# Optimization experiments

Hardware: AMD Instinct MI355X
Metric: run time of the kernel (lower is better)

Reference implementation:

```python
import jax, jax.numpy as jnp
import numpy as np

D_MODEL = 1024
NHEAD = 16
D_FF = 4096
LN_EPS = 1e-5


def _layer_norm(x, g, b):
    mu = jnp.mean(x, axis=-1, keepdims=True)
    var = jnp.mean(jnp.square(x - mu), axis=-1, keepdims=True)
    return (x - mu) * jax.lax.rsqrt(var + LN_EPS) * g + b


def setup_inputs() -> dict:
    key = jax.random.key(0)
    ks = jax.random.split(key, 12)
    d, f = D_MODEL, D_FF
    s = 1.0 / np.sqrt(d)
    inp = {
        "src": jax.random.normal(ks[0], (2, 2048, d), dtype=jnp.float32),
        "Wq": jax.random.uniform(ks[1], (d, d), jnp.float32, -s, s),
        "bq": jnp.zeros((d,), jnp.float32),
        "Wk": jax.random.uniform(ks[2], (d, d), jnp.float32, -s, s),
        "bk": jnp.zeros((d,), jnp.float32),
        "Wv": jax.random.uniform(ks[3], (d, d), jnp.float32, -s, s),
        "bv": jnp.zeros((d,), jnp.float32),
        "Wo": jax.random.uniform(ks[4], (d, d), jnp.float32, -s, s),
        "bo": jnp.zeros((d,), jnp.float32),
        "W1": jax.random.uniform(ks[5], (d, f), jnp.float32, -s, s),
        "b1": jnp.zeros((f,), jnp.float32),
        "W2": jax.random.uniform(ks[6], (f, d), jnp.float32, -1.0 / np.sqrt(f), 1.0 / np.sqrt(f)),
        "b2": jnp.zeros((d,), jnp.float32),
        "ln1_g": jnp.ones((d,), jnp.float32),
        "ln1_b": jnp.zeros((d,), jnp.float32),
        "ln2_g": jnp.ones((d,), jnp.float32),
        "ln2_b": jnp.zeros((d,), jnp.float32),
    }
    return inp


def reference(src, Wq, bq, Wk, bk, Wv, bv, Wo, bo, W1, b1, W2, b2,
              ln1_g, ln1_b, ln2_g, ln2_b):
    B, S, D = src.shape
    H = NHEAD
    hd = D // H
    # QKV projections, split into heads: [B, H, S, hd]
    q = (src @ Wq + bq).reshape(B, S, H, hd).transpose(0, 2, 1, 3)
    k = (src @ Wk + bk).reshape(B, S, H, hd).transpose(0, 2, 1, 3)
    v = (src @ Wv + bv).reshape(B, S, H, hd).transpose(0, 2, 1, 3)
    # Explicit full-score attention (no mask branch), as in source.
    scores = jnp.einsum("bhqd,bhkd->bhqk", q, k) / jnp.sqrt(jnp.asarray(hd, src.dtype))
    attn = jax.nn.softmax(scores, axis=-1)
    ctx = jnp.einsum("bhqk,bhkd->bhqd", attn, v)
    ctx = ctx.transpose(0, 2, 1, 3).reshape(B, S, D)
    src2 = ctx @ Wo + bo
    x = _layer_norm(src + src2, ln1_g, ln1_b)
    ff = jax.nn.relu(x @ W1 + b1) @ W2 + b2
    out = _layer_norm(x + ff, ln2_g, ln2_b)
    return out
```

## Files before the change

kernel.cpp:

```cpp
#include <hip/hip_runtime.h>
#include <cstdint>
#include <cstddef>

#define SEQ 2048
#define BATCH 2
#define ROWS (BATCH * SEQ)

typedef __attribute__((ext_vector_type(8))) short short8;
typedef __attribute__((ext_vector_type(4))) float f32x4;
typedef __attribute__((ext_vector_type(16))) float f32x16;
typedef __attribute__((ext_vector_type(8))) _Float16 half8;
typedef __attribute__((ext_vector_type(2))) __fp16 fp16x2;

__device__ __forceinline__ unsigned short f2bf(float f) {
  union { float f; uint32_t u; } v; v.f = f;
  uint32_t r = v.u + 0x7fffu + ((v.u >> 16) & 1u);
  return (unsigned short)(r >> 16);
}

__device__ __forceinline__ unsigned short bf2h(unsigned short b) {
  union { uint32_t u; float f; } v; v.u = ((uint32_t)b) << 16;
  union { _Float16 h; unsigned short u; } o; o.h = (_Float16)v.f;
  return o.u;
}

__device__ __forceinline__ void async16(const void* g, void* l) {
  __builtin_amdgcn_global_load_lds((const __attribute__((address_space(1))) void*)g,
                                   (__attribute__((address_space(3))) void*)l, 16, 0, 0);
}

__global__ __launch_bounds__(256) void f2bf_kernel(const float* __restrict__ in,
                                                   unsigned short* __restrict__ out) {
  size_t i = ((size_t)blockIdx.x * 256 + threadIdx.x) * 4;
  float4 vv = *(const float4*)(in + i);
  ushort4 o;
  o.x = f2bf(vv.x); o.y = f2bf(vv.y); o.z = f2bf(vv.z); o.w = f2bf(vv.w);
  *(ushort4*)(out + i) = o;
}

__global__ __launch_bounds__(256) void wtrans(const float* __restrict__ W,
                                              unsigned short* __restrict__ WT,
                                              int K, int N, float scale) {
  __shared__ float t[32][33];
  int n0 = blockIdx.x * 32, k0 = blockIdx.y * 32;
  for (int i = threadIdx.y; i < 32; i += 8)
    t[i][threadIdx.x] = W[(size_t)(k0 + i) * N + n0 + threadIdx.x];
  __syncthreads();
  for (int i = threadIdx.y; i < 32; i += 8)
    WT[(size_t)(n0 + i) * K + k0 + threadIdx.x] = f2bf(t[threadIdx.x][i] * scale);
}

__global__ __launch_bounds__(256) void bias_concat(const float* __restrict__ bq,
                                                   const float* __restrict__ bk,
                                                   const float* __restrict__ bv,
                                                   float* __restrict__ o) {
  int i = blockIdx.x * 256 + threadIdx.x;
  float v = (i < 1024) ? bq[i] * 0.18033688f : (i < 2048 ? bk[i - 1024] : bv[i - 2048]);
  o[i] = v;
}

__global__ __launch_bounds__(256) void vtrans(const unsigned short* __restrict__ qkv,
                                              unsigned short* __restrict__ VT) {
  const int st = blockIdx.x, bh = blockIdx.y, b = bh >> 4, h = bh & 15;
  __shared__ unsigned short t[64][72];
  const int tid = threadIdx.x;
#pragma unroll
  for (int it = 0; it < 2; ++it) {
    int i = it * 256 + tid;
    int s = i >> 3, c = (i & 7) * 8;
    short8 v = *(const short8*)(qkv + ((size_t)b * SEQ + st * 64 + s) * 3072 + 2048 + h * 64 + c);
#pragma unroll
    for (int j = 0; j < 8; ++j) t[c + j][s] = bf2h((unsigned short)v[j]);
  }
  __syncthreads();
#pragma unroll
  for (int it = 0; it < 2; ++it) {
    int i = it * 256 + tid;
    int d = i >> 3, sc = (i & 7) * 8;
    short8 o;
#pragma unroll
    for (int j = 0; j < 8; ++j) o[j] = (short)t[d][sc + j];
    *(short8*)(VT + ((size_t)bh * 64 + d) * 2048 + st * 64 + sc) = o;
  }
}

template <bool RELU>
__global__ __launch_bounds__(512, 2) void gemm_8p(
    const unsigned short* __restrict__ A, const unsigned short* __restrict__ BT,
    const float* __restrict__ bias, unsigned short* __restrict__ outB,
    int M, int N, int K) {
  __shared__ __align__(16) unsigned short lds[65536];
  const int tid = threadIdx.x;
  const int lane = tid & 63, ln = lane & 15, quad = lane >> 4;
  const int wid = tid >> 6, wm = wid >> 2, wn = wid & 3;
  const int m0 = blockIdx.y * 256, n0 = blockIdx.x * 256;
  const int srow = tid >> 2, scol = (tid & 3) * 8;
  const unsigned short* Ag0 = A + (size_t)(m0 + srow) * K + scol;
  const unsigned short* Ag1 = A + (size_t)(m0 + srow + 128) * K + scol;
  const unsigned short* Bg0 = BT + (size_t)(n0 + srow) * K + scol;
  const unsigned short* Bg1 = BT + (size_t)(n0 + srow + 128) * K + scol;
  const int sdst = tid * 8;
  f32x4 acc[8][4] = {};
  short8 fa[2][4];
  short8 fb[2][4];
  const int NT = K >> 6;
#pragma unroll
  for (int kh = 0; kh < 2; ++kh) {
    async16(Ag0 + kh * 32, &lds[kh * 8192 + sdst]);
    async16(Ag1 + kh * 32, &lds[kh * 8192 + sdst + 4096]);
    async16(Bg0 + kh * 32, &lds[16384 + kh * 8192 + sdst]);
    async16(Bg1 + kh * 32, &lds[16384 + kh * 8192 + sdst + 4096]);
  }
  asm volatile("s_waitcnt vmcnt(0)" ::: "memory");
  __builtin_amdgcn_s_barrier();
  {
    const unsigned short* ab = &lds[0];
#pragma unroll
    for (int fi = 0; fi < 4; ++fi)
      fa[1][fi] = *(const short8*)&ab[(wm * 128 + fi * 16 + ln) * 32 + quad * 8];
#pragma unroll
    for (int ni = 0; ni < 4; ++ni)
      fb[0][ni] = *(const short8*)&ab[16384 + (wn * 64 + ni * 16 + ln) * 32 + quad * 8];
  }
  for (int t = 0; t < NT; ++t) {
    const int cb = (t & 1) * 32768, nb = cb ^ 32768;
    const bool more = (t + 1 < NT);
    const int knext = (t + 1) * 64;
#pragma unroll
    for (int p = 0; p < 4; ++p) {
      if (p < 3) {
        const int kk2 = (p + 1) >> 1, mh2 = (p + 1) & 1;
        const unsigned short* ab = &lds[cb + kk2 * 8192];
#pragma unroll
        for (int fi = 0; fi < 4; ++fi)
          fa[p & 1][fi] =
              *(const short8*)&ab[(wm * 128 + mh2 * 64 + fi * 16 + ln) * 32 + quad * 8];
        if (p == 1) {
#pragma unroll
          for (int ni = 0; ni < 4; ++ni)
            fb[1][ni] = *(const short8*)&ab[16384 + (wn * 64 + ni * 16 + ln) * 32 + quad * 8];
        }
      } else if (more) {
        const unsigned short* ab = &lds[nb];
#pragma unroll
        for (int fi = 0; fi < 4; ++fi)
          fa[1][fi] = *(const short8*)&ab[(wm * 128 + fi * 16 + ln) * 32 + quad * 8];
#pragma unroll
        for (int ni = 0; ni < 4; ++ni)
          fb[0][ni] = *(const short8*)&ab[16384 + (wn * 64 + ni * 16 + ln) * 32 + quad * 8];
      }
      if (more && p < 2) {
        unsigned short* d = &lds[nb + p * 8192];
        async16(Ag0 + knext + p * 32, d + sdst);
        async16(Ag1 + knext + p * 32, d + sdst + 4096);
        async16(Bg0 + knext + p * 32, d + 16384 + sdst);
        async16(Bg1 + knext + p * 32, d + 16384 + sdst + 4096);
      }
      if (p == 0) {
        if (more) asm volatile("s_waitcnt vmcnt(4)" ::: "memory");
        else      asm volatile("s_waitcnt vmcnt(0)" ::: "memory");
      } else if (p == 2 && more) {
        asm volatile("s_waitcnt vmcnt(4)" ::: "memory");
      }
      __builtin_amdgcn_s_barrier();
      __builtin_amdgcn_s_setprio(1);
#pragma unroll
      for (int fi = 0; fi < 4; ++fi)
#pragma unroll
        for (int ni = 0; ni < 4; ++ni)
          acc[(p & 1) * 4 + fi][ni] = __builtin_amdgcn_mfma_f32_16x16x32_bf16(
              fa[(p + 1) & 1][fi], fb[p >> 1][ni], acc[(p & 1) * 4 + fi][ni], 0, 0, 0);
      __builtin_amdgcn_s_setprio(0);
      if (p < 3 || more) __builtin_amdgcn_s_barrier();
    }
  }
#pragma unroll
  for (int mi = 0; mi < 8; ++mi)
#pragma unroll
    for (int ni = 0; ni < 4; ++ni)
#pragma unroll
      for (int reg = 0; reg < 4; ++reg) {
        int row = m0 + wm * 128 + mi * 16 + quad * 4 + reg;
        int col = n0 + wn * 64 + ni * 16 + ln;
        float v = acc[mi][ni][reg] + bias[col];
        if (RELU) v = fmaxf(v, 0.f);
        outB[(size_t)row * N + col] = f2bf(v);
      }
}

template <bool RELU, bool OUTBF, bool HASRES>
__global__ __launch_bounds__(256) void gemm_bt64(
    const unsigned short* __restrict__ A, const unsigned short* __restrict__ BT,
    const float* __restrict__ bias, const float* __restrict__ Rres,
    float* __restrict__ outF, unsigned short* __restrict__ outB,
    int M, int N, int K) {
  __shared__ unsigned short As[4][128 * 32];
  __shared__ unsigned short Bs[4][64 * 32];
  const int tid = threadIdx.x;
  const int lane = tid & 63, ln = lane & 15, quad = lane >> 4;
  const int w = tid >> 6;
  const int m0 = blockIdx.y * 128, n0 = blockIdx.x * 64;
  const int mw = w * 32;
  f32x4 acc[2][4] = {};
  const int i0 = tid, i1 = tid + 256;
  const int r0 = i0 >> 2, kc0 = (i0 & 3) * 8;
  const int r1 = i1 >> 2, kc1 = (i1 & 3) * 8;
  for (int k0 = 0; k0 < K; k0 += 128) {
    __syncthreads();
#pragma unroll
    for (int p = 0; p < 4; ++p) {
      const int kp = k0 + p * 32;
      async16(A + (size_t)(m0 + r0) * K + kp + kc0, &As[p][i0 * 8]);
      async16(A + (size_t)(m0 + r1) * K + kp + kc1, &As[p][i1 * 8]);
      async16(BT + (size_t)(n0 + r0) * K + kp + kc0, &Bs[p][i0 * 8]);
    }
    __syncthreads();
#pragma unroll
    for (int p = 0; p < 4; ++p) {
      short8 a[2], b[4];
#pragma unroll
      for (int mi = 0; mi < 2; ++mi)
        a[mi] = *(const short8*)&As[p][(mw + mi * 16 + ln) * 32 + quad * 8];
#pragma unroll
      for (int ni = 0; ni < 4; ++ni)
        b[ni] = *(const short8*)&Bs[p][(ni * 16 + ln) * 32 + quad * 8];
#pragma unroll
      for (int mi = 0; mi < 2; ++mi)
#pragma unroll
        for (int ni = 0; ni < 4; ++ni)
          acc[mi][ni] = __builtin_amdgcn_mfma_f32_16x16x32_bf16(a[mi], b[ni], acc[mi][ni], 0, 0, 0);
    }
  }
#pragma unroll
  for (int mi = 0; mi < 2; ++mi) {
#pragma unroll
    for (int ni = 0; ni < 4; ++ni) {
#pragma unroll
      for (int reg = 0; reg < 4; ++reg) {
        int row = m0 + mw + mi * 16 + quad * 4 + reg;
        int col = n0 + ni * 16 + ln;
        float v = acc[mi][ni][reg] + bias[col];
        if (HASRES) v += Rres[(size_t)row * N + col];
        if (RELU) v = fmaxf(v, 0.f);
        if (OUTBF) outB[(size_t)row * N + col] = f2bf(v);
        else outF[(size_t)row * N + col] = v;
      }
    }
  }
}

__global__ __launch_bounds__(128, 2) void attn_kernel(const unsigned short* __restrict__ qkv,
                                                      const unsigned short* __restrict__ VT,
                                                      unsigned short* __restrict__ ctx) {
  const int qt = blockIdx.x;
  const int bh = blockIdx.y, b = bh >> 4, h = bh & 15;
  const int tid = threadIdx.x;
  const int w = tid >> 6, lane = tid & 63;
  const int r32 = lane & 31, hi = lane >> 5, r7 = r32 & 7;
  __shared__ __align__(16) unsigned short Ks[2 * 4096];
  __shared__ __align__(16) unsigned short Vs[2 * 4096];
  const size_t rowbase = (size_t)b * SEQ;
  const unsigned short* kbase = qkv + rowbase * 3072 + 1024 + h * 64;
  const unsigned short* vbase = VT + (size_t)bh * 64 * 2048;
  int r_[4], s_[4], wsw_[4];
#pragma unroll
  for (int i = 0; i < 4; ++i) {
    int idx = i * 128 + tid;
    r_[i] = idx >> 3; s_[i] = idx & 7;
    wsw_[i] = r_[i] * 64 + ((s_[i] ^ (r_[i] & 7)) * 8);
  }
  short8 qf[4];
  {
    const unsigned short* qp = qkv + (rowbase + qt * 64 + w * 32 + r32) * 3072 + h * 64;
#pragma unroll
    for (int dc = 0; dc < 4; ++dc) qf[dc] = *(const short8*)(qp + dc * 16 + hi * 8);
  }
  short8 kst[4], vst[4];
#pragma unroll
  for (int i = 0; i < 4; ++i) {
    kst[i] = *(const short8*)(kbase + (size_t)r_[i] * 3072 + s_[i] * 8);
    vst[i] = *(const short8*)(vbase + (size_t)r_[i] * 2048 + s_[i] * 8);
  }
#pragma unroll
  for (int i = 0; i < 4; ++i) {
    *(short8*)&Ks[wsw_[i]] = kst[i];
    *(short8*)&Vs[wsw_[i]] = vst[i];
  }
  __syncthreads();
  f32x16 oacc0 = {}, oacc1 = {};
  float lsum = 0.f;
  int cur = 0;
  for (int kt = 0; kt < 32; ++kt) {
    if (kt < 31) {
      const unsigned short* kp = kbase + (size_t)(kt + 1) * 64 * 3072;
      const unsigned short* vp = vbase + (kt + 1) * 64;
#pragma unroll
      for (int i = 0; i < 4; ++i) {
        kst[i] = *(const short8*)(kp + (size_t)r_[i] * 3072 + s_[i] * 8);
        vst[i] = *(const short8*)(vp + (size_t)r_[i] * 2048 + s_[i] * 8);
      }
    }
    const unsigned short* Kb = &Ks[cur];
    const unsigned short* Vb = &Vs[cur];
    f32x16 z0 = {}, z1 = {};
    __builtin_amdgcn_s_setprio(1);
#pragma unroll
    for (int dc = 0; dc < 4; ++dc) {
      const int sl = ((dc * 2 + hi) ^ r7) * 8;
      short8 kf0 = *(const short8*)&Kb[r32 * 64 + sl];
      short8 kf1 = *(const short8*)&Kb[(32 + r32) * 64 + sl];
      z0 = __builtin_amdgcn_mfma_f32_32x32x16_bf16(kf0, qf[dc], z0, 0, 0, 0);
      z1 = __builtin_amdgcn_mfma_f32_32x32x16_bf16(kf1, qf[dc], z1, 0, 0, 0);
    }
    __builtin_amdgcn_s_setprio(0);
    half8 pf[4];
#pragma unroll
    for (int kc = 0; kc < 4; ++kc) {
      float e[8];
#pragma unroll
      for (int j = 0; j < 8; ++j) {
        float zz = (kc < 2) ? z0[(kc & 1) * 8 + j] : z1[(kc & 1) * 8 + j];
        e[j] = __builtin_amdgcn_exp2f(zz);
        lsum += e[j];
      }
      union { fp16x2 hh; unsigned int u; } a0, a1, b0, b1;
      a0.hh = __builtin_amdgcn_cvt_pkrtz(e[0], e[1]);
      a1.hh = __builtin_amdgcn_cvt_pkrtz(e[2], e[3]);
      b0.hh = __builtin_amdgcn_cvt_pkrtz(e[4], e[5]);
      b1.hh = __builtin_amdgcn_cvt_pkrtz(e[6], e[7]);
      asm volatile("v_permlane32_swap_b32 %0, %1" : "+v"(a0.u), "+v"(b0.u));
      asm volatile("v_permlane32_swap_b32 %0, %1" : "+v"(a1.u), "+v"(b1.u));
      union { unsigned int u[4]; half8 hh; } fr;
      fr.u[0] = a0.u; fr.u[1] = a1.u; fr.u[2] = b0.u; fr.u[3] = b1.u;
      pf[kc] = fr.hh;
    }
    __builtin_amdgcn_s_setprio(1);
#pragma unroll
    for (int kc = 0; kc < 4; ++kc) {
      const int sl = ((kc * 2 + hi) ^ r7) * 8;
      half8 vf0 = *(const half8*)&Vb[r32 * 64 + sl];
      half8 vf1 = *(const half8*)&Vb[(32 + r32) * 64 + sl];
      oacc0 = __builtin_amdgcn_mfma_f32_32x32x16_f16(vf0, pf[kc], oacc0, 0, 0, 0);
      oacc1 = __builtin_amdgcn_mfma_f32_32x32x16_f16(vf1, pf[kc], oacc1, 0, 0, 0);
    }
    __builtin_amdgcn_s_setprio(0);
    if (kt < 31) {
      const int nb = cur ^ 4096;
#pragma unroll
      for (int i = 0; i < 4; ++i) {
        *(short8*)&Ks[nb + wsw_[i]] = kst[i];
        *(short8*)&Vs[nb + wsw_[i]] = vst[i];
      }
      __syncthreads();
      cur = nb;
    }
  }
  float tot = lsum + __shfl_xor(lsum, 32);
  float rl = 1.0f / tot;
  const size_t orow = (rowbase + (size_t)qt * 64 + w * 32 + r32) * 1024 + h * 64 + hi * 4;
#pragma unroll
  for (int tq = 0; tq < 4; ++tq) {
    ushort4 o0, o1;
    o0.x = f2bf(oacc0[tq * 4 + 0] * rl); o0.y = f2bf(oacc0[tq * 4 + 1] * rl);
    o0.z = f2bf(oacc0[tq * 4 + 2] * rl); o0.w = f2bf(oacc0[tq * 4 + 3] * rl);
    *(ushort4*)(ctx + orow + tq * 8) = o0;
    o1.x = f2bf(oacc1[tq * 4 + 0] * rl); o1.y = f2bf(oacc1[tq * 4 + 1] * rl);
    o1.z = f2bf(oacc1[tq * 4 + 2] * rl); o1.w = f2bf(oacc1[tq * 4 + 3] * rl);
    *(ushort4*)(ctx + orow + 32 + tq * 8) = o1;
  }
}

__global__ __launch_bounds__(256) void ln_kernel(const float* __restrict__ y,
                                                 const float* __restrict__ g,
                                                 const float* __restrict__ bb,
                                                 float* __restrict__ outF,
                                                 unsigned short* __restrict__ outB) {
  const int row = blockIdx.x;
  const int tid = threadIdx.x;
  const float* yr = y + (size_t)row * 1024;
  float v[4]; float s = 0.f, s2 = 0.f;
#pragma unroll
  for (int j = 0; j < 4; ++j) {
    v[j] = yr[tid + j * 256];
    s += v[j]; s2 += v[j] * v[j];
  }
#pragma unroll
  for (int off = 1; off < 64; off <<= 1) {
    s += __shfl_xor(s, off);
    s2 += __shfl_xor(s2, off);
  }
  __shared__ float ws1[4], ws2[4];
  if ((tid & 63) == 0) { ws1[tid >> 6] = s; ws2[tid >> 6] = s2; }
  __syncthreads();
  s = ws1[0] + ws1[1] + ws1[2] + ws1[3];
  s2 = ws2[0] + ws2[1] + ws2[2] + ws2[3];
  const float mu = s * (1.f / 1024.f);
  const float var = s2 * (1.f / 1024.f) - mu * mu;
  const float rstd = rsqrtf(var + 1e-5f);
#pragma unroll
  for (int j = 0; j < 4; ++j) {
    int c = tid + j * 256;
    float val = (v[j] - mu) * rstd * g[c] + bb[c];
    if (outF) outF[(size_t)row * 1024 + c] = val;
    if (outB) outB[(size_t)row * 1024 + c] = f2bf(val);
  }
}

extern "C" void kernel_launch(void* const* d_in, const int* in_sizes, int n_in,
                              void* d_out, int out_size, void* d_ws, size_t ws_size,
                              hipStream_t stream) {
  const float* src = (const float*)d_in[0];
  const float* Wq = (const float*)d_in[1];
  const float* bq = (const float*)d_in[2];
  const float* Wk = (const float*)d_in[3];
  const float* bk = (const float*)d_in[4];
  const float* Wv = (const float*)d_in[5];
  const float* bv = (const float*)d_in[6];
  const float* Wo = (const float*)d_in[7];
  const float* bo = (const float*)d_in[8];
  const float* W1 = (const float*)d_in[9];
  const float* b1 = (const float*)d_in[10];
  const float* W2 = (const float*)d_in[11];
  const float* b2 = (const float*)d_in[12];
  const float* ln1g = (const float*)d_in[13];
  const float* ln1b = (const float*)d_in[14];
  const float* ln2g = (const float*)d_in[15];
  const float* ln2b = (const float*)d_in[16];
  float* out = (float*)d_out;

  char* ws = (char*)d_ws;
  unsigned short* qkvT = (unsigned short*)(ws + 0);
  unsigned short* WoT  = (unsigned short*)(ws + 6291456);
  unsigned short* W1T  = (unsigned short*)(ws + 8388608);
  unsigned short* W2T  = (unsigned short*)(ws + 16777216);
  float*          biasq = (float*)(ws + 25165824);
  unsigned short* xbf  = (unsigned short*)(ws + 25178112);
  unsigned short* qkv  = (unsigned short*)(ws + 33566720);
  unsigned short* hbuf = qkv;
  unsigned short* ctx  = (unsigned short*)(ws + 58732544);
  float*          ybuf = (float*)(ws + 67121152);
  unsigned short* VT   = (unsigned short*)(ws + 67121152);
  float*          xf   = (float*)(ws + 83898368);

  const float QSCALE = 0.18033688f;

  f2bf_kernel<<<4096, 256, 0, stream>>>(src, xbf);
  wtrans<<<dim3(32, 32), dim3(32, 8), 0, stream>>>(Wq, qkvT, 1024, 1024, QSCALE);
  wtrans<<<dim3(32, 32), dim3(32, 8), 0, stream>>>(Wk, qkvT + 1024 * 1024, 1024, 1024, 1.0f);
  wtrans<<<dim3(32, 32), dim3(32, 8), 0, stream>>>(Wv, qkvT + 2048 * 1024, 1024, 1024, 1.0f);
  wtrans<<<dim3(32, 32), dim3(32, 8), 0, stream>>>(Wo, WoT, 1024, 1024, 1.0f);
  wtrans<<<dim3(128, 32), dim3(32, 8), 0, stream>>>(W1, W1T, 1024, 4096, 1.0f);
  wtrans<<<dim3(32, 128), dim3(32, 8), 0, stream>>>(W2, W2T, 4096, 1024, 1.0f);
  bias_concat<<<12, 256, 0, stream>>>(bq, bk, bv, biasq);

  gemm_8p<false><<<dim3(12, 16), 512, 0, stream>>>(xbf, qkvT, biasq, qkv, ROWS, 3072, 1024);
  vtrans<<<dim3(32, 32), 256, 0, stream>>>(qkv, VT);
  attn_kernel<<<dim3(32, 32), 128, 0, stream>>>(qkv, VT, ctx);
  gemm_bt64<false, false, true><<<dim3(16, 32), 256, 0, stream>>>(
      ctx, WoT, bo, src, ybuf, nullptr, ROWS, 1024, 1024);
  ln_kernel<<<4096, 256, 0, stream>>>(ybuf, ln1g, ln1b, xf, xbf);
  gemm_8p<true><<<dim3(16, 16), 512, 0, stream>>>(xbf, W1T, b1, hbuf, ROWS, 4096, 1024);
  gemm_bt64<false, false, true><<<dim3(16, 32), 256, 0, stream>>>(
      hbuf, W2T, b2, xf, ybuf, nullptr, ROWS, 1024, 4096);
  ln_kernel<<<4096, 256, 0, stream>>>(ybuf, ln2g, ln2b, out, nullptr);
}
```

Baseline: 373.8 us.

## Merge prep kernels into one launch and extend attention LDS swizzle

Replaces eight preprocessing launches (input bf16 cast, six weight transposes, bias concat) with one prep_kernel that dispatches on block index, cutting launch overhead and the gaps between small kernels. Separately, the attention kernel's K/V LDS swizzle now also XORs in bits 3-4 of the row, to reduce bank conflicts on the 32x32 MFMA fragment reads. The merged kernel adds per-block branching and divisions, and the swizzle change adds a little index arithmetic.

```diff
diff --git a/kernel.cpp b/kernel.cpp
--- a/kernel.cpp
+++ b/kernel.cpp
@@ -29,34 +29,46 @@
                                    (__attribute__((address_space(3))) void*)l, 16, 0, 0);
 }
 
-__global__ __launch_bounds__(256) void f2bf_kernel(const float* __restrict__ in,
-                                                   unsigned short* __restrict__ out) {
-  size_t i = ((size_t)blockIdx.x * 256 + threadIdx.x) * 4;
-  float4 vv = *(const float4*)(in + i);
-  ushort4 o;
-  o.x = f2bf(vv.x); o.y = f2bf(vv.y); o.z = f2bf(vv.z); o.w = f2bf(vv.w);
-  *(ushort4*)(out + i) = o;
-}
-
-__global__ __launch_bounds__(256) void wtrans(const float* __restrict__ W,
-                                              unsigned short* __restrict__ WT,
-                                              int K, int N, float scale) {
-  __shared__ float t[32][33];
-  int n0 = blockIdx.x * 32, k0 = blockIdx.y * 32;
-  for (int i = threadIdx.y; i < 32; i += 8)
-    t[i][threadIdx.x] = W[(size_t)(k0 + i) * N + n0 + threadIdx.x];
-  __syncthreads();
-  for (int i = threadIdx.y; i < 32; i += 8)
-    WT[(size_t)(n0 + i) * K + k0 + threadIdx.x] = f2bf(t[threadIdx.x][i] * scale);
-}
-
-__global__ __launch_bounds__(256) void bias_concat(const float* __restrict__ bq,
-                                                   const float* __restrict__ bk,
-                                                   const float* __restrict__ bv,
-                                                   float* __restrict__ o) {
-  int i = blockIdx.x * 256 + threadIdx.x;
-  float v = (i < 1024) ? bq[i] * 0.18033688f : (i < 2048 ? bk[i - 1024] : bv[i - 2048]);
-  o[i] = v;
+__global__ __launch_bounds__(256) void prep_kernel(
+    const float* __restrict__ src,
+    const float* __restrict__ Wq, const float* __restrict__ Wk,
+    const float* __restrict__ Wv, const float* __restrict__ Wo,
+    const float* __restrict__ W1, const float* __restrict__ W2,
+    const float* __restrict__ bq, const float* __restrict__ bk,
+    const float* __restrict__ bv,
+    unsigned short* __restrict__ qkvT, unsigned short* __restrict__ WoT,
+    unsigned short* __restrict__ W1T, unsigned short* __restrict__ W2T,
+    float* __restrict__ biasq, unsigned short* __restrict__ xbf) {
+  const int blk = blockIdx.x;
+  if (blk < 12288) {
+    const float* W; unsigned short* WT; int K, N, nbx, base; float scale = 1.0f;
+    if (blk < 1024)      { W = Wq; WT = qkvT;             K = 1024; N = 1024; nbx = 32;  base = 0;    scale = 0.18033688f; }
+    else if (blk < 2048) { W = Wk; WT = qkvT + 1048576;   K = 1024; N = 1024; nbx = 32;  base = 1024; }
+    else if (blk < 3072) { W = Wv; WT = qkvT + 2097152;   K = 1024; N = 1024; nbx = 32;  base = 2048; }
+    else if (blk < 4096) { W = Wo; WT = WoT;              K = 1024; N = 1024; nbx = 32;  base = 3072; }
+    else if (blk < 8192) { W = W1; WT = W1T;              K = 1024; N = 4096; nbx = 128; base = 4096; }
+    else                 { W = W2; WT = W2T;              K = 4096; N = 1024; nbx = 32;  base = 8192; }
+    const int lb = blk - base;
+    const int bx = lb % nbx, by = lb / nbx;
+    __shared__ float t[32][33];
+    const int tx = threadIdx.x & 31, ty = threadIdx.x >> 5;
+    const int n0 = bx * 32, k0 = by * 32;
+    for (int i = ty; i < 32; i += 8)
+      t[i][tx] = W[(size_t)(k0 + i) * N + n0 + tx];
+    __syncthreads();
+    for (int i = ty; i < 32; i += 8)
+      WT[(size_t)(n0 + i) * K + k0 + tx] = f2bf(t[tx][i] * scale);
+  } else if (blk < 12300) {
+    int i = (blk - 12288) * 256 + threadIdx.x;
+    float v = (i < 1024) ? bq[i] * 0.18033688f : (i < 2048 ? bk[i - 1024] : bv[i - 2048]);
+    biasq[i] = v;
+  } else {
+    size_t i = ((size_t)(blk - 12300) * 256 + threadIdx.x) * 4;
+    float4 vv = *(const float4*)(src + i);
+    ushort4 o;
+    o.x = f2bf(vv.x); o.y = f2bf(vv.y); o.z = f2bf(vv.z); o.w = f2bf(vv.w);
+    *(ushort4*)(xbf + i) = o;
+  }
 }
 
 __global__ __launch_bounds__(256) void vtrans(const unsigned short* __restrict__ qkv,
@@ -257,6 +269,7 @@
   const int tid = threadIdx.x;
   const int w = tid >> 6, lane = tid & 63;
   const int r32 = lane & 31, hi = lane >> 5, r7 = r32 & 7;
+  const int sw2 = (r32 >> 3) & 3;
   __shared__ __align__(16) unsigned short Ks[2 * 4096];
   __shared__ __align__(16) unsigned short Vs[2 * 4096];
   const size_t rowbase = (size_t)b * SEQ;
@@ -267,7 +280,7 @@
   for (int i = 0; i < 4; ++i) {
     int idx = i * 128 + tid;
     r_[i] = idx >> 3; s_[i] = idx & 7;
-    wsw_[i] = r_[i] * 64 + ((s_[i] ^ (r_[i] & 7)) * 8);
+    wsw_[i] = r_[i] * 64 + ((s_[i] ^ (r_[i] & 7) ^ ((r_[i] >> 3) & 3)) * 8);
   }
   short8 qf[4];
   {
@@ -306,7 +319,7 @@
     __builtin_amdgcn_s_setprio(1);
 #pragma unroll
     for (int dc = 0; dc < 4; ++dc) {
-      const int sl = ((dc * 2 + hi) ^ r7) * 8;
+      const int sl = (((dc * 2 + hi) ^ r7 ^ sw2) & 7) * 8;
       short8 kf0 = *(const short8*)&Kb[r32 * 64 + sl];
       short8 kf1 = *(const short8*)&Kb[(32 + r32) * 64 + sl];
       z0 = __builtin_amdgcn_mfma_f32_32x32x16_bf16(kf0, qf[dc], z0, 0, 0, 0);
@@ -337,7 +350,7 @@
     __builtin_amdgcn_s_setprio(1);
 #pragma unroll
     for (int kc = 0; kc < 4; ++kc) {
-      const int sl = ((kc * 2 + hi) ^ r7) * 8;
+      const int sl = (((kc * 2 + hi) ^ r7 ^ sw2) & 7) * 8;
       half8 vf0 = *(const half8*)&Vb[r32 * 64 + sl];
       half8 vf1 = *(const half8*)&Vb[(32 + r32) * 64 + sl];
       oacc0 = __builtin_amdgcn_mfma_f32_32x32x16_f16(vf0, pf[kc], oacc0, 0, 0, 0);
@@ -442,16 +455,8 @@
   unsigned short* VT   = (unsigned short*)(ws + 67121152);
   float*          xf   = (float*)(ws + 83898368);
 
-  const float QSCALE = 0.18033688f;
-
-  f2bf_kernel<<<4096, 256, 0, stream>>>(src, xbf);
-  wtrans<<<dim3(32, 32), dim3(32, 8), 0, stream>>>(Wq, qkvT, 1024, 1024, QSCALE);
-  wtrans<<<dim3(32, 32), dim3(32, 8), 0, stream>>>(Wk, qkvT + 1024 * 1024, 1024, 1024, 1.0f);
-  wtrans<<<dim3(32, 32), dim3(32, 8), 0, stream>>>(Wv, qkvT + 2048 * 1024, 1024, 1024, 1.0f);
-  wtrans<<<dim3(32, 32), dim3(32, 8), 0, stream>>>(Wo, WoT, 1024, 1024, 1.0f);
-  wtrans<<<dim3(128, 32), dim3(32, 8), 0, stream>>>(W1, W1T, 1024, 4096, 1.0f);
-  wtrans<<<dim3(32, 128), dim3(32, 8), 0, stream>>>(W2, W2T, 4096, 1024, 1.0f);
-  bias_concat<<<12, 256, 0, stream>>>(bq, bk, bv, biasq);
+  prep_kernel<<<16396, 256, 0, stream>>>(src, Wq, Wk, Wv, Wo, W1, W2, bq, bk, bv,
+                                         qkvT, WoT, W1T, W2T, biasq, xbf);
 
   gemm_8p<false><<<dim3(12, 16), 512, 0, stream>>>(xbf, qkvT, biasq, qkv, ROWS, 3072, 1024);
   vtrans<<<dim3(32, 32), 256, 0, stream>>>(qkv, VT);
```

Result: faster. 365.9 us, median of 2 (-2.1%).
